# Kernel tuning notes

Hardware: AMD Instinct MI355X
Metric: run time of the kernel (lower is better)

The kernel has to match this reference:

```python
import jax, jax.numpy as jnp
import numpy as np

N_QUBITS = 4
DIM = 1 << N_QUBITS  # 16


def _apply1(state, gate, q):
    # state: [B, 16] complex; gate: [2,2] or [B,2,2]; q: qubit index (0 = MSB)
    B = state.shape[0]
    left = 1 << q
    right = 1 << (N_QUBITS - q - 1)
    s = state.reshape(B, left, 2, right)
    if gate.ndim == 2:
        out = jnp.einsum('ij,bajc->baic', gate, s)
    else:
        out = jnp.einsum('bij,bajc->baic', gate, s)
    return out.reshape(B, DIM)


def _cnot(state, c, t):
    # flip target axis where control bit == 1
    B = state.shape[0]
    s = state.reshape((B,) + (2,) * N_QUBITS)
    s0 = jax.lax.index_in_dim(s, 0, c + 1, keepdims=True)
    s1 = jax.lax.index_in_dim(s, 1, c + 1, keepdims=True)
    s1 = jnp.flip(s1, axis=t + 1)
    return jnp.concatenate([s0, s1], axis=c + 1).reshape(B, DIM)


def _ry(theta):
    # theta: [B] -> [B,2,2] complex
    c = jnp.cos(theta / 2)
    s = jnp.sin(theta / 2)
    g = jnp.stack([jnp.stack([c, -s], -1), jnp.stack([s, c], -1)], -2)
    return g.astype(jnp.complex64)


def _rz(theta):
    e0 = jnp.exp(-1j * theta.astype(jnp.complex64) / 2)
    e1 = jnp.exp(1j * theta.astype(jnp.complex64) / 2)
    z = jnp.zeros_like(e0)
    return jnp.stack([jnp.stack([e0, z], -1), jnp.stack([z, e1], -1)], -2)


def _u3(theta, phi, lam):
    # scalar params -> [2,2] complex
    th = theta.astype(jnp.complex64)
    ph = phi.astype(jnp.complex64)
    la = lam.astype(jnp.complex64)
    c = jnp.cos(th / 2)
    s = jnp.sin(th / 2)
    return jnp.array([[1.0, 0.0], [0.0, 0.0]], jnp.complex64) * c \
        + jnp.array([[0.0, -1.0], [0.0, 0.0]], jnp.complex64) * (jnp.exp(1j * la) * s) \
        + jnp.array([[0.0, 0.0], [1.0, 0.0]], jnp.complex64) * (jnp.exp(1j * ph) * s) \
        + jnp.array([[0.0, 0.0], [0.0, 1.0]], jnp.complex64) * (jnp.exp(1j * (ph + la)) * c)


_H = (jnp.array([[1.0, 1.0], [1.0, -1.0]], jnp.float32) / np.sqrt(2.0)).astype(jnp.complex64)


def _circuit(ry_ang, rz_ang, u3_params):
    # ry_ang, rz_ang: [B, 4]; u3_params: [4, 3]
    B = ry_ang.shape[0]
    state = jnp.zeros((B, DIM), jnp.complex64).at[:, 0].set(1.0)
    for q in range(N_QUBITS):
        state = _apply1(state, _H, q)
    for q in range(N_QUBITS):
        state = _apply1(state, _ry(ry_ang[:, q]), q)
    for q in range(N_QUBITS):
        state = _apply1(state, _rz(rz_ang[:, q]), q)
    for q in range(N_QUBITS):  # cnot_ring step=1
        state = _cnot(state, q, (q + 1) % N_QUBITS)
    for q in range(N_QUBITS):  # cnot_ring step=2
        state = _cnot(state, q, (q + 2) % N_QUBITS)
    for q in range(N_QUBITS):
        state = _apply1(state, _u3(u3_params[q, 0], u3_params[q, 1], u3_params[q, 2]), q)
    # Z expectations on each wire
    probs = jnp.abs(state) ** 2  # [B, 16]
    probs = probs.reshape((B,) + (2,) * N_QUBITS)
    exps = []
    for q in range(N_QUBITS):
        axes = tuple(a for a in range(1, N_QUBITS + 1) if a != q + 1)
        p = jnp.sum(probs, axis=axes)  # [B, 2]
        exps.append(p[:, 0] - p[:, 1])
    return jnp.stack(exps, axis=1)  # [B, 4]


def setup_inputs() -> dict:
    key = jax.random.key(0)
    k = jax.random.split(key, 6)
    B = 32768
    input_features = jax.random.normal(k[0], (B, 512), jnp.float32)
    pre_w = jax.random.normal(k[1], (N_QUBITS, 512), jnp.float32) / np.sqrt(512.0)
    pre_b = jnp.zeros((N_QUBITS,), jnp.float32)
    u3_params = jax.random.uniform(k[2], (N_QUBITS, 3), jnp.float32, 0.0, 2.0 * np.pi)
    post_w = jax.random.normal(k[3], (2, N_QUBITS), jnp.float32) / np.sqrt(float(N_QUBITS))
    post_b = jnp.zeros((2,), jnp.float32)
    return {"input_features": input_features, "pre_w": pre_w, "pre_b": pre_b,
            "u3_params": u3_params, "post_w": post_w, "post_b": post_b}


def reference(input_features, pre_w, pre_b, u3_params, post_w, post_b):
    pre_out = input_features @ pre_w.T + pre_b              # [B, 4]
    q_in = jnp.tanh(pre_out / 10.0) * (np.pi / 2.0)          # [B, 4]
    ry_ang = jnp.arctan(q_in)
    rz_ang = jnp.arctan(q_in * q_in)
    q_out = _circuit(ry_ang, rz_ang, u3_params)              # [B, 4] real
    return q_out @ post_w.T + post_b                         # [B, 2]
```

## Files before the change

kernel.cpp:

```cpp
#include <hip/hip_runtime.h>
#include <math.h>

#define NQ 4
#define DIM 16
#define K 512

__global__ __launch_bounds__(256) void qnet_gemm(const float* __restrict__ x,
                                                 const float* __restrict__ w,
                                                 const float* __restrict__ bias,
                                                 float* __restrict__ pre_out,
                                                 int B) {
    int wave = (int)((blockIdx.x * blockDim.x + threadIdx.x) >> 6);
    int lane = (int)(threadIdx.x & 63);
    if (wave >= B) return;

    const float* xr = x + (size_t)wave * K;
    float4 x0 = *(const float4*)(xr + lane * 4);
    float4 x1 = *(const float4*)(xr + 256 + lane * 4);

    float acc[NQ];
#pragma unroll
    for (int q = 0; q < NQ; ++q) {
        const float* wr = w + q * K;
        float4 w0 = *(const float4*)(wr + lane * 4);
        float4 w1 = *(const float4*)(wr + 256 + lane * 4);
        acc[q] = x0.x * w0.x + x0.y * w0.y + x0.z * w0.z + x0.w * w0.w
               + x1.x * w1.x + x1.y * w1.y + x1.z * w1.z + x1.w * w1.w;
    }

#pragma unroll
    for (int off = 32; off >= 1; off >>= 1) {
#pragma unroll
        for (int q = 0; q < NQ; ++q)
            acc[q] += __shfl_xor(acc[q], off, 64);
    }

    if (lane == 0) {
        float4 r = make_float4(acc[0] + bias[0], acc[1] + bias[1],
                               acc[2] + bias[2], acc[3] + bias[3]);
        *(float4*)(pre_out + (size_t)wave * 4) = r;
    }
}

__global__ __launch_bounds__(64) void qnet_circuit(const float* __restrict__ pre_out,
                                                   const float* __restrict__ u3p,
                                                   const float* __restrict__ post_w,
                                                   const float* __restrict__ post_b,
                                                   float* __restrict__ out,
                                                   int B) {
    int b = (int)(blockIdx.x * blockDim.x + threadIdx.x);
    if (b >= B) return;

    float4 p4 = *(const float4*)(pre_out + (size_t)b * 4);
    float pre[NQ] = {p4.x, p4.y, p4.z, p4.w};

    float ry[NQ], rz[NQ];
#pragma unroll
    for (int q = 0; q < NQ; ++q) {
        float qi = tanhf(pre[q] * 0.1f) * 1.5707963267948966f;
        ry[q] = atanf(qi);
        rz[q] = atanf(qi * qi);
    }

    float sr[DIM], si[DIM];
#pragma unroll
    for (int i = 0; i < DIM; ++i) { sr[i] = 0.25f; si[i] = 0.0f; }

#pragma unroll
    for (int q = 0; q < NQ; ++q) {
        float c, s;
        __sincosf(ry[q] * 0.5f, &s, &c);
        const int m = 1 << (3 - q);
#pragma unroll
        for (int i = 0; i < DIM; ++i) {
            if (i & m) continue;
            const int j = i | m;
            float r0 = sr[i], i0 = si[i], r1 = sr[j], i1 = si[j];
            sr[i] = c * r0 - s * r1;  si[i] = c * i0 - s * i1;
            sr[j] = s * r0 + c * r1;  si[j] = s * i0 + c * i1;
        }
    }

#pragma unroll
    for (int q = 0; q < NQ; ++q) {
        float c, s;
        __sincosf(rz[q] * 0.5f, &s, &c);
        const int m = 1 << (3 - q);
#pragma unroll
        for (int i = 0; i < DIM; ++i) {
            const float sg = (i & m) ? s : -s;
            float r = sr[i], im = si[i];
            sr[i] = c * r - sg * im;
            si[i] = c * im + sg * r;
        }
    }

    const int cn_c[8] = {0, 1, 2, 3, 0, 1, 2, 3};
    const int cn_t[8] = {1, 2, 3, 0, 2, 3, 0, 1};
#pragma unroll
    for (int k = 0; k < 8; ++k) {
        const int cm = 1 << (3 - cn_c[k]);
        const int tm = 1 << (3 - cn_t[k]);
#pragma unroll
        for (int i = 0; i < DIM; ++i) {
            if ((i & cm) && !(i & tm)) {
                const int j = i | tm;
                float tr = sr[i]; sr[i] = sr[j]; sr[j] = tr;
                float ti = si[i]; si[i] = si[j]; si[j] = ti;
            }
        }
    }

#pragma unroll
    for (int q = 0; q < NQ; ++q) {
        float th = u3p[q * 3 + 0], ph = u3p[q * 3 + 1], la = u3p[q * 3 + 2];
        float ct, st, cl, sl, cp, sp, cpl, spl;
        __sincosf(th * 0.5f, &st, &ct);
        __sincosf(la, &sl, &cl);
        __sincosf(ph, &sp, &cp);
        __sincosf(ph + la, &spl, &cpl);
        const float g01r = -cl * st, g01i = -sl * st;
        const float g10r = cp * st,  g10i = sp * st;
        const float g11r = cpl * ct, g11i = spl * ct;
        const int m = 1 << (3 - q);
#pragma unroll
        for (int i = 0; i < DIM; ++i) {
            if (i & m) continue;
            const int j = i | m;
            float r0 = sr[i], i0 = si[i], r1 = sr[j], i1 = si[j];
            sr[i] = ct * r0 + g01r * r1 - g01i * i1;
            si[i] = ct * i0 + g01r * i1 + g01i * r1;
            sr[j] = g10r * r0 - g10i * i0 + g11r * r1 - g11i * i1;
            si[j] = g10r * i0 + g10i * r0 + g11r * i1 + g11i * r1;
        }
    }

    float ex[NQ] = {0.f, 0.f, 0.f, 0.f};
#pragma unroll
    for (int i = 0; i < DIM; ++i) {
        const float p2 = sr[i] * sr[i] + si[i] * si[i];
#pragma unroll
        for (int q = 0; q < NQ; ++q)
            ex[q] += (i & (1 << (3 - q))) ? -p2 : p2;
    }

    float o0 = post_b[0], o1 = post_b[1];
#pragma unroll
    for (int q = 0; q < NQ; ++q) {
        o0 += ex[q] * post_w[q];
        o1 += ex[q] * post_w[4 + q];
    }
    *(float2*)(out + (size_t)b * 2) = make_float2(o0, o1);
}

extern "C" void kernel_launch(void* const* d_in, const int* in_sizes, int n_in,
                              void* d_out, int out_size, void* d_ws, size_t ws_size,
                              hipStream_t stream) {
    const float* x      = (const float*)d_in[0];
    const float* pre_w  = (const float*)d_in[1];
    const float* pre_b  = (const float*)d_in[2];
    const float* u3p    = (const float*)d_in[3];
    const float* post_w = (const float*)d_in[4];
    const float* post_b = (const float*)d_in[5];
    float* out = (float*)d_out;

    const int B = in_sizes[0] / K;
    float* pre_out = (float*)d_ws;

    {
        int waves_per_block = 4;
        int blocks = (B + waves_per_block - 1) / waves_per_block;
        qnet_gemm<<<blocks, waves_per_block * 64, 0, stream>>>(x, pre_w, pre_b, pre_out, B);
    }
    {
        int threads = 64;
        int blocks = (B + threads - 1) / threads;
        qnet_circuit<<<blocks, threads, 0, stream>>>(pre_out, u3p, post_w, post_b, out, B);
    }
}
```

Measured before the change: 103.2 us.

## Process four rows per wave in GEMM with transpose-style shuffle reduction

Each wave in the projection kernel now handles four input rows and loads the weight vectors once into registers, reusing them across rows. The cross-lane reduction swaps partial sums between lanes so that each lane carries one row/qubit value, which cuts the number of shuffles, and 16 lanes write the results. The circuit kernel uses 256-thread blocks and replaces tanhf with an exp-based formula, which is cheaper but may differ slightly in accuracy. The GEMM is bound by reading the 64 MB input, so the reuse and shuffle savings may matter little.

After: 103.4 us. About the same (+0.2%).

```diff
diff --git a/kernel.cpp b/kernel.cpp
--- a/kernel.cpp
+++ b/kernel.cpp
@@ -10,44 +10,71 @@
                                                  const float* __restrict__ bias,
                                                  float* __restrict__ pre_out,
                                                  int B) {
-    int wave = (int)((blockIdx.x * blockDim.x + threadIdx.x) >> 6);
-    int lane = (int)(threadIdx.x & 63);
-    if (wave >= B) return;
-
-    const float* xr = x + (size_t)wave * K;
-    float4 x0 = *(const float4*)(xr + lane * 4);
-    float4 x1 = *(const float4*)(xr + 256 + lane * 4);
-
-    float acc[NQ];
-#pragma unroll
-    for (int q = 0; q < NQ; ++q) {
-        const float* wr = w + q * K;
-        float4 w0 = *(const float4*)(wr + lane * 4);
-        float4 w1 = *(const float4*)(wr + 256 + lane * 4);
-        acc[q] = x0.x * w0.x + x0.y * w0.y + x0.z * w0.z + x0.w * w0.w
-               + x1.x * w1.x + x1.y * w1.y + x1.z * w1.z + x1.w * w1.w;
-    }
-
-#pragma unroll
-    for (int off = 32; off >= 1; off >>= 1) {
-#pragma unroll
-        for (int q = 0; q < NQ; ++q)
-            acc[q] += __shfl_xor(acc[q], off, 64);
-    }
-
-    if (lane == 0) {
-        float4 r = make_float4(acc[0] + bias[0], acc[1] + bias[1],
-                               acc[2] + bias[2], acc[3] + bias[3]);
-        *(float4*)(pre_out + (size_t)wave * 4) = r;
+    const int wid  = (int)((blockIdx.x * blockDim.x + threadIdx.x) >> 6);
+    const int lane = (int)(threadIdx.x & 63);
+    const int row0 = wid * 4;
+    if (row0 >= B) return;
+
+    float4 wf[NQ][2];
+#pragma unroll
+    for (int q = 0; q < NQ; ++q) {
+#pragma unroll
+        for (int h = 0; h < 2; ++h)
+            wf[q][h] = *(const float4*)(w + q * K + h * 256 + lane * 4);
+    }
+
+    float acc[4][NQ];
+#pragma unroll
+    for (int r = 0; r < 4; ++r) {
+        int row = row0 + r;
+        if (row >= B) row = B - 1;
+        const float* xr = x + (size_t)row * K;
+        float4 x0 = *(const float4*)(xr + lane * 4);
+        float4 x1 = *(const float4*)(xr + 256 + lane * 4);
+#pragma unroll
+        for (int q = 0; q < NQ; ++q) {
+            acc[r][q] = x0.x * wf[q][0].x + x0.y * wf[q][0].y
+                      + x0.z * wf[q][0].z + x0.w * wf[q][0].w
+                      + x1.x * wf[q][1].x + x1.y * wf[q][1].y
+                      + x1.z * wf[q][1].z + x1.w * wf[q][1].w;
+        }
+    }
+
+    const int l1 = lane & 1;
+    const int l2 = lane & 2;
+    float v[4];
+#pragma unroll
+    for (int r = 0; r < 4; ++r) {
+        float a01k = l1 ? acc[r][1] : acc[r][0];
+        float a01s = l1 ? acc[r][0] : acc[r][1];
+        a01k += __shfl_xor(a01s, 1, 64);
+        float a23k = l1 ? acc[r][3] : acc[r][2];
+        float a23s = l1 ? acc[r][2] : acc[r][3];
+        a23k += __shfl_xor(a23s, 1, 64);
+        float vk = l2 ? a23k : a01k;
+        float vs = l2 ? a01k : a23k;
+        vk += __shfl_xor(vs, 2, 64);
+#pragma unroll
+        for (int off = 4; off <= 32; off <<= 1)
+            vk += __shfl_xor(vk, off, 64);
+        v[r] = vk;
+    }
+
+    if (lane < 16) {
+        const int r = lane >> 2;
+        const int q = lane & 3;
+        float vr = (r == 0) ? v[0] : (r == 1) ? v[1] : (r == 2) ? v[2] : v[3];
+        const int row = row0 + r;
+        if (row < B) pre_out[(size_t)row * 4 + q] = vr + bias[q];
     }
 }
 
-__global__ __launch_bounds__(64) void qnet_circuit(const float* __restrict__ pre_out,
-                                                   const float* __restrict__ u3p,
-                                                   const float* __restrict__ post_w,
-                                                   const float* __restrict__ post_b,
-                                                   float* __restrict__ out,
-                                                   int B) {
+__global__ __launch_bounds__(256) void qnet_circuit(const float* __restrict__ pre_out,
+                                                    const float* __restrict__ u3p,
+                                                    const float* __restrict__ post_w,
+                                                    const float* __restrict__ post_b,
+                                                    float* __restrict__ out,
+                                                    int B) {
     int b = (int)(blockIdx.x * blockDim.x + threadIdx.x);
     if (b >= B) return;
 
@@ -57,7 +84,9 @@
     float ry[NQ], rz[NQ];
 #pragma unroll
     for (int q = 0; q < NQ; ++q) {
-        float qi = tanhf(pre[q] * 0.1f) * 1.5707963267948966f;
+        float z = pre[q] * 0.1f;
+        float t = 1.0f - 2.0f / (__expf(2.0f * z) + 1.0f);
+        float qi = t * 1.5707963267948966f;
         ry[q] = atanf(qi);
         rz[q] = atanf(qi * qi);
     }
@@ -168,12 +197,12 @@
     float* pre_out = (float*)d_ws;
 
     {
-        int waves_per_block = 4;
-        int blocks = (B + waves_per_block - 1) / waves_per_block;
-        qnet_gemm<<<blocks, waves_per_block * 64, 0, stream>>>(x, pre_w, pre_b, pre_out, B);
+        int rows_per_block = 16;
+        int blocks = (B + rows_per_block - 1) / rows_per_block;
+        qnet_gemm<<<blocks, 256, 0, stream>>>(x, pre_w, pre_b, pre_out, B);
     }
     {
-        int threads = 64;
+        int threads = 256;
         int blocks = (B + threads - 1) / threads;
         qnet_circuit<<<blocks, threads, 0, stream>>>(pre_out, u3p, post_w, post_b, out, B);
     }
```
